# Performance work log

Hardware: AMD Instinct MI355X
Metric: run time of the kernel (lower is better)

The kernel has to match this reference:

```python
import jax, jax.numpy as jnp
import numpy as np

N_NODES = 10000
N_EDGES = 640000
IN_FEATS = 256
H_FEATS = 128
NUM_CLASSES = 64


def _kaiming(key, shape):
    fan_in = shape[1]
    std = np.sqrt(2.0 / fan_in)
    return jax.random.normal(key, shape, dtype=jnp.float32) * std


def setup_inputs() -> dict:
    key = jax.random.key(0)
    ks = jax.random.split(key, 10)
    x = jax.random.normal(ks[0], (N_NODES, IN_FEATS), dtype=jnp.float32)
    edge_index = jax.random.randint(ks[1], (2, N_EDGES), 0, N_NODES, dtype=jnp.int64)
    return {
        "x": x,
        "edge_index": edge_index,
        "W_lin": _kaiming(ks[2], (H_FEATS, IN_FEATS)),
        "b_lin": jnp.zeros((H_FEATS,), jnp.float32),
        "Wl1": _kaiming(ks[3], (H_FEATS, H_FEATS)),
        "bl1": jnp.zeros((H_FEATS,), jnp.float32),
        "Wr1": _kaiming(ks[4], (H_FEATS, H_FEATS)),
        "Wl2": _kaiming(ks[5], (H_FEATS, H_FEATS)),
        "bl2": jnp.zeros((H_FEATS,), jnp.float32),
        "Wr2": _kaiming(ks[6], (H_FEATS, H_FEATS)),
        "W_cls": _kaiming(ks[7], (NUM_CLASSES, H_FEATS)),
    }


def _sage_conv(x, src, dst, Wl, bl, Wr, n_nodes):
    # PyG SAGEConv (mean aggr): out = lin_l(mean_{j->i} x_j) + lin_r(x_i)
    msg = x[src]                                    # [E, H] gather
    agg = jax.ops.segment_sum(msg, dst, num_segments=n_nodes)  # [N, H]
    deg = jax.ops.segment_sum(jnp.ones((src.shape[0],), x.dtype), dst,
                              num_segments=n_nodes)            # [N]
    mean = agg / jnp.maximum(deg, 1.0)[:, None]
    return mean @ Wl.T + bl + x @ Wr.T


def reference(x, edge_index, W_lin, b_lin, Wl1, bl1, Wr1, Wl2, bl2, Wr2, W_cls):
    src, dst = edge_index[0], edge_index[1]
    n = x.shape[0]
    h = jax.nn.relu(x @ W_lin.T + b_lin)            # input projection + relu
    h = _sage_conv(h, src, dst, Wl1, bl1, Wr1, n)   # sage1 (no relu: linear is truthy)
    h = _sage_conv(h, src, dst, Wl2, bl2, Wr2, n)   # sage2
    h = jax.nn.relu(h)
    return h @ W_cls.T                              # weight.mm(x.t()).t()
```

## Files before the change

### kernel.cpp

```cpp
#include <hip/hip_runtime.h>

#define NN 10000
#define HF 128
#define INF_ 256
#define CLS 64
#define CAP 128
#define RT  (NN / 16)

typedef __attribute__((ext_vector_type(8))) short short8;
typedef __attribute__((ext_vector_type(4))) float f32x4;

__device__ __forceinline__ unsigned short f2bf(float f) {
    unsigned u = __builtin_bit_cast(unsigned, f);
    u = (u + 0x7fffu + ((u >> 16) & 1u)) >> 16;
    return (unsigned short)u;
}
__device__ __forceinline__ float bfbits2f(unsigned u) {
    u <<= 16;
    return __builtin_bit_cast(float, u);
}


template <int K>
__device__ __forceinline__
void mfma_acc(int row_tile, int col0,
              const unsigned short* __restrict__ A,
              const unsigned short* __restrict__ W, f32x4 acc[4]) {
    int lane = threadIdx.x & 63;
    int m = lane & 15, quad = lane >> 4;
    const short8* ap  = (const short8*)(A + (size_t)(row_tile * 16 + m) * K + quad * 8);
    const short8* bp0 = (const short8*)(W + (size_t)(col0 +  0 + m) * K + quad * 8);
    const short8* bp1 = (const short8*)(W + (size_t)(col0 + 16 + m) * K + quad * 8);
    const short8* bp2 = (const short8*)(W + (size_t)(col0 + 32 + m) * K + quad * 8);
    const short8* bp3 = (const short8*)(W + (size_t)(col0 + 48 + m) * K + quad * 8);
#pragma unroll
    for (int k0 = 0; k0 < K; k0 += 32) {
        int ki = k0 >> 3;
        short8 a = ap[ki];
        acc[0] = __builtin_amdgcn_mfma_f32_16x16x32_bf16(a, bp0[ki], acc[0], 0, 0, 0);
        acc[1] = __builtin_amdgcn_mfma_f32_16x16x32_bf16(a, bp1[ki], acc[1], 0, 0, 0);
        acc[2] = __builtin_amdgcn_mfma_f32_16x16x32_bf16(a, bp2[ki], acc[2], 0, 0, 0);
        acc[3] = __builtin_amdgcn_mfma_f32_16x16x32_bf16(a, bp3[ki], acc[3], 0, 0, 0);
    }
}

template <bool OUT_BF16, bool RELU_OUT, bool HAS_BIAS>
__device__ __forceinline__
void epilogue4(int row_tile, int col0, int N, const float* __restrict__ bias,
               f32x4 acc[4], void* __restrict__ out) {
    int lane = threadIdx.x & 63;
    int m = lane & 15, quad = lane >> 4;
#pragma unroll
    for (int c = 0; c < 4; ++c) {
        int colg = col0 + c * 16 + m;
        float bv = HAS_BIAS ? bias[colg] : 0.f;
#pragma unroll
        for (int r = 0; r < 4; ++r) {
            int rowg = row_tile * 16 + quad * 4 + r;
            float v = acc[c][r] + bv;
            if (RELU_OUT) v = fmaxf(v, 0.f);
            if (OUT_BF16) ((unsigned short*)out)[(size_t)rowg * N + colg] = f2bf(v);
            else          ((float*)out)[(size_t)rowg * N + colg] = v;
        }
    }
}

__device__ __forceinline__ short8 pack8(float4 a, float4 b) {
    short8 r;
    r[0] = (short)f2bf(a.x); r[1] = (short)f2bf(a.y);
    r[2] = (short)f2bf(a.z); r[3] = (short)f2bf(a.w);
    r[4] = (short)f2bf(b.x); r[5] = (short)f2bf(b.y);
    r[6] = (short)f2bf(b.z); r[7] = (short)f2bf(b.w);
    return r;
}

__device__ __forceinline__
void gemm1_wave(int row_tile, int col0, const float* __restrict__ x,
                const float* __restrict__ Wlin, const float* __restrict__ blin,
                unsigned short* __restrict__ h0) {
    int lane = threadIdx.x & 63;
    int m = lane & 15, quad = lane >> 4;
    const float* ar = x    + (size_t)(row_tile * 16 + m) * INF_ + quad * 8;
    const float* w0 = Wlin + (size_t)(col0 +  0 + m) * INF_ + quad * 8;
    const float* w1 = Wlin + (size_t)(col0 + 16 + m) * INF_ + quad * 8;
    const float* w2 = Wlin + (size_t)(col0 + 32 + m) * INF_ + quad * 8;
    const float* w3 = Wlin + (size_t)(col0 + 48 + m) * INF_ + quad * 8;
    f32x4 acc[4] = {};
#pragma unroll
    for (int k0 = 0; k0 < INF_; k0 += 32) {
        short8 a  = pack8(*(const float4*)(ar + k0), *(const float4*)(ar + k0 + 4));
        short8 b0 = pack8(*(const float4*)(w0 + k0), *(const float4*)(w0 + k0 + 4));
        short8 b1 = pack8(*(const float4*)(w1 + k0), *(const float4*)(w1 + k0 + 4));
        short8 b2 = pack8(*(const float4*)(w2 + k0), *(const float4*)(w2 + k0 + 4));
        short8 b3 = pack8(*(const float4*)(w3 + k0), *(const float4*)(w3 + k0 + 4));
        acc[0] = __builtin_amdgcn_mfma_f32_16x16x32_bf16(a, b0, acc[0], 0, 0, 0);
        acc[1] = __builtin_amdgcn_mfma_f32_16x16x32_bf16(a, b1, acc[1], 0, 0, 0);
        acc[2] = __builtin_amdgcn_mfma_f32_16x16x32_bf16(a, b2, acc[2], 0, 0, 0);
        acc[3] = __builtin_amdgcn_mfma_f32_16x16x32_bf16(a, b3, acc[3], 0, 0, 0);
    }
    epilogue4<true, true, true>(row_tile, col0, HF, blin, acc, h0);
}

#define GB 313
#define FB 2500
#define CB 288

__global__ __launch_bounds__(256)
void fused_k(const float* __restrict__ x, const float* __restrict__ Wlin,
             const float* __restrict__ blin, unsigned short* __restrict__ h0,
             const int* __restrict__ src, const int* __restrict__ dst,
             int* __restrict__ cnt, unsigned short* __restrict__ colb, int E,
             const float* __restrict__ Wl1, const float* __restrict__ Wr1,
             const float* __restrict__ Wl2, const float* __restrict__ Wr2,
             const float* __restrict__ Wcls, unsigned short* __restrict__ wb) {
    int b = blockIdx.x;
    if (b < GB) {
        int wave = threadIdx.x >> 6;
        int row_tile = b * 2 + (wave >> 1);
        if (row_tile >= RT) return;
        gemm1_wave(row_tile, (wave & 1) * 64, x, Wlin, blin, h0);
    } else if (b < GB + FB) {
        int i = (b - GB) * 256 + threadIdx.x;
        if (i < E) {
            int d = dst[i];
            int pos = atomicAdd(&cnt[d], 1);
            if (pos < CAP) colb[(size_t)d * CAP + pos] = (unsigned short)src[i];
        }
    } else {
        int i = (b - GB - FB) * 256 + threadIdx.x;
        const float* s; int off;
        if      (i < 16384) { s = Wl1;  off = 0; }
        else if (i < 32768) { s = Wr1;  off = 16384; }
        else if (i < 49152) { s = Wl2;  off = 32768; }
        else if (i < 65536) { s = Wr2;  off = 49152; }
        else if (i < 73728) { s = Wcls; off = 65536; }
        else return;
        wb[i] = f2bf(s[i - off]);
    }
}

__global__ __launch_bounds__(256)
void agg_kernel(const unsigned short* __restrict__ h, const int* __restrict__ cnt,
                const unsigned short* __restrict__ colb,
                unsigned short* __restrict__ mv, int n) {
    int wave = threadIdx.x >> 6;
    int lane = threadIdx.x & 63;
    int half = lane >> 5;
    int l32  = lane & 31;
    int node = blockIdx.x * 4 + wave;
    if (node >= n) return;
    int deg = cnt[node];
    int c = deg > CAP ? CAP : deg;
    const unsigned short* mycol = colb + (size_t)node * CAP;
    const uint2* __restrict__ hp = (const uint2*)h;

    float s0f = 0.f, s1f = 0.f, s2f = 0.f, s3f = 0.f;
    float t0f = 0.f, t1f = 0.f, t2f = 0.f, t3f = 0.f;
    for (int base = 0; base < c; base += 64) {
        int mm = min(64, c - base);
        int colv = (base + lane < c) ? (int)mycol[base + lane] : 0;
        for (int j = 0; j < mm; j += 4) {
            int e0 = j + half;
            int e1 = j + 2 + half;
            int i0 = __shfl(colv, e0);
            int i1 = __shfl(colv, e1);
            if (e0 < mm) {
                uint2 v = hp[(size_t)i0 * 32 + l32];
                s0f += bfbits2f(v.x & 0xffffu); s1f += bfbits2f(v.x >> 16);
                s2f += bfbits2f(v.y & 0xffffu); s3f += bfbits2f(v.y >> 16);
            }
            if (e1 < mm) {
                uint2 v = hp[(size_t)i1 * 32 + l32];
                t0f += bfbits2f(v.x & 0xffffu); t1f += bfbits2f(v.x >> 16);
                t2f += bfbits2f(v.y & 0xffffu); t3f += bfbits2f(v.y >> 16);
            }
        }
    }
    s0f += t0f; s1f += t1f; s2f += t2f; s3f += t3f;
    s0f += __shfl_xor(s0f, 32);
    s1f += __shfl_xor(s1f, 32);
    s2f += __shfl_xor(s2f, 32);
    s3f += __shfl_xor(s3f, 32);
    if (half == 0) {
        float inv = (deg > 0) ? 1.0f / (float)deg : 0.f;
        uint2 o;
        o.x = (unsigned)f2bf(s0f * inv) | ((unsigned)f2bf(s1f * inv) << 16);
        o.y = (unsigned)f2bf(s2f * inv) | ((unsigned)f2bf(s3f * inv) << 16);
        ((uint2*)mv)[(size_t)node * 32 + l32] = o;
    }
}

template <bool RELU_OUT>
__global__ __launch_bounds__(256)
void sage_gemm_k(const unsigned short* __restrict__ mv, const unsigned short* __restrict__ Wl,
                 const unsigned short* __restrict__ h,  const unsigned short* __restrict__ Wr,
                 const float* __restrict__ bias, unsigned short* __restrict__ out) {
    int wave = threadIdx.x >> 6;
    int row_tile = blockIdx.x * 2 + (wave >> 1);
    if (row_tile >= RT) return;
    int col0 = (wave & 1) * 64;
    f32x4 acc[4] = {};
    mfma_acc<HF>(row_tile, col0, mv, Wl, acc);
    mfma_acc<HF>(row_tile, col0, h,  Wr, acc);
    epilogue4<true, RELU_OUT, true>(row_tile, col0, HF, bias, acc, out);
}

__global__ __launch_bounds__(256)
void cls_gemm_k(const unsigned short* __restrict__ h2r,
                const unsigned short* __restrict__ Wc, float* __restrict__ out) {
    int wave = threadIdx.x >> 6;
    int row_tile = blockIdx.x * 4 + wave;
    if (row_tile >= RT) return;
    f32x4 acc[4] = {};
    mfma_acc<HF>(row_tile, 0, h2r, Wc, acc);
    epilogue4<false, false, false>(row_tile, 0, CLS, nullptr, acc, out);
}


extern "C" void kernel_launch(void* const* d_in, const int* in_sizes, int n_in,
                              void* d_out, int out_size, void* d_ws, size_t ws_size,
                              hipStream_t stream) {
    const float* x      = (const float*)d_in[0];
    const int*   ei     = (const int*)d_in[1];
    const float* W_lin  = (const float*)d_in[2];
    const float* b_lin  = (const float*)d_in[3];
    const float* Wl1    = (const float*)d_in[4];
    const float* bl1    = (const float*)d_in[5];
    const float* Wr1    = (const float*)d_in[6];
    const float* Wl2    = (const float*)d_in[7];
    const float* bl2    = (const float*)d_in[8];
    const float* Wr2    = (const float*)d_in[9];
    const float* W_cls  = (const float*)d_in[10];
    float* out = (float*)d_out;

    const int E = in_sizes[1] / 2;
    const int* src = ei;
    const int* dst = ei + E;

    unsigned short* wb  = (unsigned short*)d_ws;
    unsigned short* wbl1 = wb;
    unsigned short* wbr1 = wb + 16384;
    unsigned short* wbl2 = wb + 32768;
    unsigned short* wbr2 = wb + 49152;
    unsigned short* wbc  = wb + 65536;
    unsigned short* h0  = wb + 73728;
    unsigned short* mv  = h0 + (size_t)NN * HF;
    unsigned short* h1  = mv + (size_t)NN * HF;
    unsigned short* h2r = h1 + (size_t)NN * HF;
    int* cnt = (int*)(h2r + (size_t)NN * HF);
    unsigned short* colb = (unsigned short*)(cnt + NN);

    hipMemsetAsync(cnt, 0, NN * sizeof(int), stream);

    fused_k<<<GB + FB + CB, 256, 0, stream>>>(
        x, W_lin, b_lin, h0, src, dst, cnt, colb, E,
        Wl1, Wr1, Wl2, Wr2, W_cls, wb);

    agg_kernel<<<(NN + 3) / 4, 256, 0, stream>>>(h0, cnt, colb, mv, NN);
    sage_gemm_k<false><<<(RT + 1) / 2, 256, 0, stream>>>(mv, wbl1, h0, wbr1, bl1, h1);

    agg_kernel<<<(NN + 3) / 4, 256, 0, stream>>>(h1, cnt, colb, mv, NN);
    sage_gemm_k<true><<<(RT + 1) / 2, 256, 0, stream>>>(mv, wbl2, h1, wbr2, bl2, h2r);

    cls_gemm_k<<<(RT + 3) / 4, 256, 0, stream>>>(h2r, wbc, out);
}
```

Measured before the change: 192.8 us.

## Overlap root-feature GEMM with aggregation, widen gathers, vectorize CSR build

The lin_r(x_i) GEMM moves into the aggregation kernel as extra blocks that write an fp32 partial to a temp buffer, so it runs concurrently with the gather. The finishing kernel then does only the mean@Wl GEMM and adds that partial in its epilogue. The aggregation now gathers 16-byte rows with four edges per wave step instead of 8-byte loads. The edge bucketing processes four edges per thread using int4 loads. This adds an fp32 temp buffer that costs extra write and read traffic.

New measurement: 195.6 us. No clear change (+1.4%).

```diff
diff --git a/kernel.cpp b/kernel.cpp
--- a/kernel.cpp
+++ b/kernel.cpp
@@ -44,10 +44,10 @@
     }
 }
 
-template <bool OUT_BF16, bool RELU_OUT, bool HAS_BIAS>
+template <bool OUT_BF16, bool RELU_OUT, bool HAS_BIAS, bool HAS_TMP>
 __device__ __forceinline__
 void epilogue4(int row_tile, int col0, int N, const float* __restrict__ bias,
-               f32x4 acc[4], void* __restrict__ out) {
+               const float* __restrict__ tmp, f32x4 acc[4], void* __restrict__ out) {
     int lane = threadIdx.x & 63;
     int m = lane & 15, quad = lane >> 4;
 #pragma unroll
@@ -58,6 +58,7 @@
         for (int r = 0; r < 4; ++r) {
             int rowg = row_tile * 16 + quad * 4 + r;
             float v = acc[c][r] + bv;
+            if (HAS_TMP) v += tmp[(size_t)rowg * N + colg];
             if (RELU_OUT) v = fmaxf(v, 0.f);
             if (OUT_BF16) ((unsigned short*)out)[(size_t)rowg * N + colg] = f2bf(v);
             else          ((float*)out)[(size_t)rowg * N + colg] = v;
@@ -98,11 +99,11 @@
         acc[2] = __builtin_amdgcn_mfma_f32_16x16x32_bf16(a, b2, acc[2], 0, 0, 0);
         acc[3] = __builtin_amdgcn_mfma_f32_16x16x32_bf16(a, b3, acc[3], 0, 0, 0);
     }
-    epilogue4<true, true, true>(row_tile, col0, HF, blin, acc, h0);
+    epilogue4<true, true, true, false>(row_tile, col0, HF, blin, nullptr, acc, h0);
 }
 
 #define GB 313
-#define FB 2500
+#define FB 625
 #define CB 288
 
 __global__ __launch_bounds__(256)
@@ -120,11 +121,18 @@
         if (row_tile >= RT) return;
         gemm1_wave(row_tile, (wave & 1) * 64, x, Wlin, blin, h0);
     } else if (b < GB + FB) {
-        int i = (b - GB) * 256 + threadIdx.x;
-        if (i < E) {
-            int d = dst[i];
-            int pos = atomicAdd(&cnt[d], 1);
-            if (pos < CAP) colb[(size_t)d * CAP + pos] = (unsigned short)src[i];
+        int t = (b - GB) * 256 + threadIdx.x;
+        if (t * 4 < E) {
+            int4 s4 = ((const int4*)src)[t];
+            int4 d4 = ((const int4*)dst)[t];
+            int p0 = atomicAdd(&cnt[d4.x], 1);
+            int p1 = atomicAdd(&cnt[d4.y], 1);
+            int p2 = atomicAdd(&cnt[d4.z], 1);
+            int p3 = atomicAdd(&cnt[d4.w], 1);
+            if (p0 < CAP) colb[(size_t)d4.x * CAP + p0] = (unsigned short)s4.x;
+            if (p1 < CAP) colb[(size_t)d4.y * CAP + p1] = (unsigned short)s4.y;
+            if (p2 < CAP) colb[(size_t)d4.z * CAP + p2] = (unsigned short)s4.z;
+            if (p3 < CAP) colb[(size_t)d4.w * CAP + p3] = (unsigned short)s4.w;
         }
     } else {
         int i = (b - GB - FB) * 256 + threadIdx.x;
@@ -139,70 +147,85 @@
     }
 }
 
-__global__ __launch_bounds__(256)
-void agg_kernel(const unsigned short* __restrict__ h, const int* __restrict__ cnt,
-                const unsigned short* __restrict__ colb,
-                unsigned short* __restrict__ mv, int n) {
-    int wave = threadIdx.x >> 6;
-    int lane = threadIdx.x & 63;
-    int half = lane >> 5;
-    int l32  = lane & 31;
-    int node = blockIdx.x * 4 + wave;
-    if (node >= n) return;
-    int deg = cnt[node];
-    int c = deg > CAP ? CAP : deg;
-    const unsigned short* mycol = colb + (size_t)node * CAP;
-    const uint2* __restrict__ hp = (const uint2*)h;
-
-    float s0f = 0.f, s1f = 0.f, s2f = 0.f, s3f = 0.f;
-    float t0f = 0.f, t1f = 0.f, t2f = 0.f, t3f = 0.f;
-    for (int base = 0; base < c; base += 64) {
-        int mm = min(64, c - base);
-        int colv = (base + lane < c) ? (int)mycol[base + lane] : 0;
-        for (int j = 0; j < mm; j += 4) {
-            int e0 = j + half;
-            int e1 = j + 2 + half;
-            int i0 = __shfl(colv, e0);
-            int i1 = __shfl(colv, e1);
-            if (e0 < mm) {
-                uint2 v = hp[(size_t)i0 * 32 + l32];
-                s0f += bfbits2f(v.x & 0xffffu); s1f += bfbits2f(v.x >> 16);
-                s2f += bfbits2f(v.y & 0xffffu); s3f += bfbits2f(v.y >> 16);
+#define AGB 2500
+
+__global__ __launch_bounds__(256)
+void agg_gemm_k(const unsigned short* __restrict__ h, const int* __restrict__ cnt,
+                const unsigned short* __restrict__ colb, unsigned short* __restrict__ mv,
+                const unsigned short* __restrict__ Wr, float* __restrict__ tmp, int n) {
+    int b = blockIdx.x;
+    if (b < AGB) {
+        int wave = threadIdx.x >> 6;
+        int lane = threadIdx.x & 63;
+        int q   = lane >> 4;
+        int r16 = lane & 15;
+        int node = b * 4 + wave;
+        if (node >= n) return;
+        int deg = cnt[node];
+        int c = deg > CAP ? CAP : deg;
+        const unsigned short* mycol = colb + (size_t)node * CAP;
+        const uint4* __restrict__ hp = (const uint4*)h;
+
+        float a0 = 0.f, a1 = 0.f, a2 = 0.f, a3 = 0.f;
+        float a4 = 0.f, a5 = 0.f, a6 = 0.f, a7 = 0.f;
+        for (int base = 0; base < c; base += 64) {
+            int mm = min(64, c - base);
+            int colv = (base + lane < c) ? (int)mycol[base + lane] : 0;
+#pragma unroll 4
+            for (int jj = 0; jj < 16; ++jj) {
+                if (jj * 4 >= mm) break;
+                int e = jj * 4 + q;
+                int s = __shfl(colv, e);
+                if (e < mm) {
+                    uint4 v = hp[(size_t)s * 16 + r16];
+                    a0 += bfbits2f(v.x & 0xffffu); a1 += bfbits2f(v.x >> 16);
+                    a2 += bfbits2f(v.y & 0xffffu); a3 += bfbits2f(v.y >> 16);
+                    a4 += bfbits2f(v.z & 0xffffu); a5 += bfbits2f(v.z >> 16);
+                    a6 += bfbits2f(v.w & 0xffffu); a7 += bfbits2f(v.w >> 16);
+                }
             }
-            if (e1 < mm) {
-                uint2 v = hp[(size_t)i1 * 32 + l32];
-                t0f += bfbits2f(v.x & 0xffffu); t1f += bfbits2f(v.x >> 16);
-                t2f += bfbits2f(v.y & 0xffffu); t3f += bfbits2f(v.y >> 16);
-            }
-        }
-    }
-    s0f += t0f; s1f += t1f; s2f += t2f; s3f += t3f;
-    s0f += __shfl_xor(s0f, 32);
-    s1f += __shfl_xor(s1f, 32);
-    s2f += __shfl_xor(s2f, 32);
-    s3f += __shfl_xor(s3f, 32);
-    if (half == 0) {
-        float inv = (deg > 0) ? 1.0f / (float)deg : 0.f;
-        uint2 o;
-        o.x = (unsigned)f2bf(s0f * inv) | ((unsigned)f2bf(s1f * inv) << 16);
-        o.y = (unsigned)f2bf(s2f * inv) | ((unsigned)f2bf(s3f * inv) << 16);
-        ((uint2*)mv)[(size_t)node * 32 + l32] = o;
+        }
+        a0 += __shfl_xor(a0, 16); a0 += __shfl_xor(a0, 32);
+        a1 += __shfl_xor(a1, 16); a1 += __shfl_xor(a1, 32);
+        a2 += __shfl_xor(a2, 16); a2 += __shfl_xor(a2, 32);
+        a3 += __shfl_xor(a3, 16); a3 += __shfl_xor(a3, 32);
+        a4 += __shfl_xor(a4, 16); a4 += __shfl_xor(a4, 32);
+        a5 += __shfl_xor(a5, 16); a5 += __shfl_xor(a5, 32);
+        a6 += __shfl_xor(a6, 16); a6 += __shfl_xor(a6, 32);
+        a7 += __shfl_xor(a7, 16); a7 += __shfl_xor(a7, 32);
+        if (q == 0) {
+            float inv = (deg > 0) ? 1.0f / (float)deg : 0.f;
+            uint4 o;
+            o.x = (unsigned)f2bf(a0 * inv) | ((unsigned)f2bf(a1 * inv) << 16);
+            o.y = (unsigned)f2bf(a2 * inv) | ((unsigned)f2bf(a3 * inv) << 16);
+            o.z = (unsigned)f2bf(a4 * inv) | ((unsigned)f2bf(a5 * inv) << 16);
+            o.w = (unsigned)f2bf(a6 * inv) | ((unsigned)f2bf(a7 * inv) << 16);
+            ((uint4*)mv)[(size_t)node * 16 + r16] = o;
+        }
+    } else {
+        int bb = b - AGB;
+        int wave = threadIdx.x >> 6;
+        int row_tile = bb * 2 + (wave >> 1);
+        if (row_tile >= RT) return;
+        int col0 = (wave & 1) * 64;
+        f32x4 acc[4] = {};
+        mfma_acc<HF>(row_tile, col0, h, Wr, acc);
+        epilogue4<false, false, false, false>(row_tile, col0, HF, nullptr, nullptr, acc, tmp);
     }
 }
 
 template <bool RELU_OUT>
 __global__ __launch_bounds__(256)
-void sage_gemm_k(const unsigned short* __restrict__ mv, const unsigned short* __restrict__ Wl,
-                 const unsigned short* __restrict__ h,  const unsigned short* __restrict__ Wr,
-                 const float* __restrict__ bias, unsigned short* __restrict__ out) {
+void sage_fin_k(const unsigned short* __restrict__ mv, const unsigned short* __restrict__ Wl,
+                const float* __restrict__ tmp, const float* __restrict__ bias,
+                unsigned short* __restrict__ out) {
     int wave = threadIdx.x >> 6;
     int row_tile = blockIdx.x * 2 + (wave >> 1);
     if (row_tile >= RT) return;
     int col0 = (wave & 1) * 64;
     f32x4 acc[4] = {};
     mfma_acc<HF>(row_tile, col0, mv, Wl, acc);
-    mfma_acc<HF>(row_tile, col0, h,  Wr, acc);
-    epilogue4<true, RELU_OUT, true>(row_tile, col0, HF, bias, acc, out);
+    epilogue4<true, RELU_OUT, true, true>(row_tile, col0, HF, bias, tmp, acc, out);
 }
 
 __global__ __launch_bounds__(256)
@@ -213,7 +236,7 @@
     if (row_tile >= RT) return;
     f32x4 acc[4] = {};
     mfma_acc<HF>(row_tile, 0, h2r, Wc, acc);
-    epilogue4<false, false, false>(row_tile, 0, CLS, nullptr, acc, out);
+    epilogue4<false, false, false, false>(row_tile, 0, CLS, nullptr, nullptr, acc, out);
 }
 
 
@@ -247,7 +270,8 @@
     unsigned short* mv  = h0 + (size_t)NN * HF;
     unsigned short* h1  = mv + (size_t)NN * HF;
     unsigned short* h2r = h1 + (size_t)NN * HF;
-    int* cnt = (int*)(h2r + (size_t)NN * HF);
+    float* tmp = (float*)(h2r + (size_t)NN * HF);
+    int* cnt = (int*)(tmp + (size_t)NN * HF);
     unsigned short* colb = (unsigned short*)(cnt + NN);
 
     hipMemsetAsync(cnt, 0, NN * sizeof(int), stream);
@@ -256,11 +280,11 @@
         x, W_lin, b_lin, h0, src, dst, cnt, colb, E,
         Wl1, Wr1, Wl2, Wr2, W_cls, wb);
 
-    agg_kernel<<<(NN + 3) / 4, 256, 0, stream>>>(h0, cnt, colb, mv, NN);
-    sage_gemm_k<false><<<(RT + 1) / 2, 256, 0, stream>>>(mv, wbl1, h0, wbr1, bl1, h1);
-
-    agg_kernel<<<(NN + 3) / 4, 256, 0, stream>>>(h1, cnt, colb, mv, NN);
-    sage_gemm_k<true><<<(RT + 1) / 2, 256, 0, stream>>>(mv, wbl2, h1, wbr2, bl2, h2r);
+    agg_gemm_k<<<AGB + 313, 256, 0, stream>>>(h0, cnt, colb, mv, wbr1, tmp, NN);
+    sage_fin_k<false><<<(RT + 1) / 2, 256, 0, stream>>>(mv, wbl1, tmp, bl1, h1);
+
+    agg_gemm_k<<<AGB + 313, 256, 0, stream>>>(h1, cnt, colb, mv, wbr2, tmp, NN);
+    sage_fin_k<true><<<(RT + 1) / 2, 256, 0, stream>>>(mv, wbl2, tmp, bl2, h2r);
 
     cls_gemm_k<<<(RT + 3) / 4, 256, 0, stream>>>(h2r, wbc, out);
 }
```
